# Kernel optimization log

Hardware: AMD Instinct MI355X
Metric: run time of the kernel (lower is better)

The kernel has to match this reference:

```python
import jax, jax.numpy as jnp
import numpy as np
from jax import lax

B, S, D, H, K = 2, 2048, 1024, 16, 3  # batch, seq, embed, heads, conv kernel
DEPTH = D // H


def silu(x):
    return x * jax.nn.sigmoid(x)


def sep_conv1d(x, dw, pw, b):
    """Keras SeparableConv1D, padding='same', activation=silu.
    x: [B,S,C]; dw: [K,1,C] depthwise kernel; pw: [C,F] pointwise; b: [F]."""
    C = x.shape[-1]
    y = lax.conv_general_dilated(
        x, dw, window_strides=(1,), padding='SAME',
        dimension_numbers=('NWC', 'WIO', 'NWC'), feature_group_count=C)
    y = jnp.einsum('bsc,cf->bsf', y, pw) + b
    return silu(y)


def setup_inputs() -> dict:
    key = jax.random.key(0)
    ks = jax.random.split(key, 20)
    sc = 1.0 / np.sqrt(D)
    inp = {
        'v': jax.random.normal(ks[0], (B, S, D), jnp.float32),
        'k': jax.random.normal(ks[1], (B, S, D), jnp.float32),
        'q': jax.random.normal(ks[2], (B, S, D), jnp.float32),
        'mask': jax.random.randint(ks[3], (B, 1, 1, S), 0, 2, jnp.int32),
        # Dense wq/wk/wv (SiLU)
        'wq_w': jax.random.normal(ks[4], (D, D), jnp.float32) * sc,
        'wq_b': jnp.zeros((D,), jnp.float32),
        'wk_w': jax.random.normal(ks[5], (D, D), jnp.float32) * sc,
        'wk_b': jnp.zeros((D,), jnp.float32),
        'wv_w': jax.random.normal(ks[6], (D, D), jnp.float32) * sc,
        'wv_b': jnp.zeros((D,), jnp.float32),
        # SeparableConv1D params (depthwise [K,1,D], pointwise [D,D], bias [D])
        'dwq': jax.random.normal(ks[7], (K, 1, D), jnp.float32) * 0.1,
        'pwq': jax.random.normal(ks[8], (D, D), jnp.float32) * sc,
        'bq': jnp.zeros((D,), jnp.float32),
        'dwk': jax.random.normal(ks[9], (K, 1, D), jnp.float32) * 0.1,
        'pwk': jax.random.normal(ks[10], (D, D), jnp.float32) * sc,
        'bk': jnp.zeros((D,), jnp.float32),
        'dwv': jax.random.normal(ks[11], (K, 1, D), jnp.float32) * 0.1,
        'pwv': jax.random.normal(ks[12], (D, D), jnp.float32) * sc,
        'bv': jnp.zeros((D,), jnp.float32),
        # output Dense (SiLU)
        'wo_w': jax.random.normal(ks[13], (D, D), jnp.float32) * sc,
        'wo_b': jnp.zeros((D,), jnp.float32),
    }
    return inp


def reference(v, k, q, mask, wq_w, wq_b, wk_w, wk_b, wv_w, wv_b,
              dwq, pwq, bq, dwk, pwk, bk, dwv, pwv, bv, wo_w, wo_b):
    # Dense projections with SiLU
    qp = silu(q @ wq_w + wq_b)
    kp = silu(k @ wk_w + wk_b)
    vp = silu(v @ wv_w + wv_b)
    # SeparableConv1D enhancements (SiLU)
    qc = sep_conv1d(qp, dwq, pwq, bq)
    kc = sep_conv1d(kp, dwk, pwk, bk)
    vc = sep_conv1d(vp, dwv, pwv, bv)
    # split heads -> [B,H,S,depth]
    def split(x):
        return x.reshape(B, S, H, DEPTH).transpose(0, 2, 1, 3)
    qh, kh, vh = split(qc), split(kc), split(vc)
    # scaled dot-product attention with additive mask penalty
    logits = jnp.einsum('bhqd,bhkd->bhqk', qh, kh) / jnp.sqrt(jnp.float32(DEPTH))
    logits = logits + mask.astype(jnp.float32) * -1e9
    attn = jax.nn.softmax(logits, axis=-1)
    out = jnp.einsum('bhqk,bhkd->bhqd', attn, vh)
    out = out.transpose(0, 2, 1, 3).reshape(B, S, D)
    return silu(out @ wo_w + wo_b)
```

## Files before the change

### kernel.cpp

```cpp
#include <hip/hip_runtime.h>
#include <hip/hip_fp16.h>
#include <math.h>

#define BB 2
#define SS 2048
#define DD 1024
#define HH 16
#define MTOT (BB*SS)

typedef _Float16 f16;
typedef _Float16 f16x4 __attribute__((ext_vector_type(4)));
typedef _Float16 f16x8 __attribute__((ext_vector_type(8)));
typedef float    f32x4 __attribute__((ext_vector_type(4)));

#define KSCALE 0.1803368801111204f

__device__ __forceinline__ float silu_f(float x) {
    return x / (1.0f + __expf(-x));
}

__device__ __forceinline__ void gload16(void* lds, const void* g) {
    __builtin_amdgcn_global_load_lds(
        (const __attribute__((address_space(1))) unsigned*)g,
        (__attribute__((address_space(3))) unsigned*)lds, 16, 0, 0);
}

__global__ __launch_bounds__(256) void prep(
    const float* __restrict__ q, const float* __restrict__ k, const float* __restrict__ v,
    f16* __restrict__ x0, f16* __restrict__ x1, f16* __restrict__ x2,
    const float* __restrict__ w0, const float* __restrict__ w1, const float* __restrict__ w2,
    const float* __restrict__ w3, const float* __restrict__ w4, const float* __restrict__ w5,
    const float* __restrict__ w6, f16* __restrict__ wt,
    const int* __restrict__ mask, int* __restrict__ uidx, int* __restrict__ ucnt)
{
    __shared__ float ts[64][65];
    const int gid = blockIdx.x;
    const int t = threadIdx.x;

    if (gid < 6144) {
        const int z = gid >> 11;
        const float* src = z == 0 ? q : z == 1 ? k : v;
        f16* dst = z == 0 ? x0 : z == 1 ? x1 : x2;
        const size_t i8 = ((size_t)(gid & 2047) * 256 + t) * 8;
        const float4 a = *(const float4*)(src + i8);
        const float4 b = *(const float4*)(src + i8 + 4);
        f16x8 h = {(f16)a.x,(f16)a.y,(f16)a.z,(f16)a.w,(f16)b.x,(f16)b.y,(f16)b.z,(f16)b.w};
        *(f16x8*)(dst + i8) = h;
    } else if (gid < 7936) {
        const int w = gid - 6144;
        const int z = w >> 8;
        const int rem = w & 255;
        const int bn = (rem & 15) << 6, bk = (rem >> 4) << 6;
        const float* src;
        switch (z) {
            case 0: src = w0; break; case 1: src = w1; break;
            case 2: src = w2; break; case 3: src = w3; break;
            case 4: src = w4; break; case 5: src = w5; break;
            default: src = w6; break;
        }
        f16* dst = wt + ((size_t)z << 20);
        #pragma unroll
        for (int i = 0; i < 4; ++i) {
            const int fid = t + (i << 8);
            const int r = fid >> 4, c4 = (fid & 15) << 2;
            const float4 v4 = *(const float4*)(src + (size_t)(bk + r) * 1024 + bn + c4);
            ts[r][c4 + 0] = v4.x; ts[r][c4 + 1] = v4.y;
            ts[r][c4 + 2] = v4.z; ts[r][c4 + 3] = v4.w;
        }
        __syncthreads();
        #pragma unroll
        for (int i = 0; i < 4; ++i) {
            const int fid = t + (i << 8);
            const int nr = fid >> 4, k4 = (fid & 15) << 2;
            f16x4 h = { (f16)ts[k4 + 0][nr], (f16)ts[k4 + 1][nr],
                        (f16)ts[k4 + 2][nr], (f16)ts[k4 + 3][nr] };
            *(f16x4*)(dst + (size_t)(bn + nr) * 1024 + bk + k4) = h;
        }
    } else {
        int* ps = (int*)ts;
        const int b = gid - 7936;
        int f[8]; int cnt = 0;
        const int base = b * SS + t * 8;
        #pragma unroll
        for (int j = 0; j < 8; ++j) { f[j] = (mask[base + j] == 0); cnt += f[j]; }
        ps[t] = cnt;
        __syncthreads();
        for (int off = 1; off < 256; off <<= 1) {
            const int pv = (t >= off) ? ps[t - off] : 0;
            __syncthreads();
            ps[t] += pv;
            __syncthreads();
        }
        int pos = ps[t] - cnt;
        #pragma unroll
        for (int j = 0; j < 8; ++j)
            if (f[j]) uidx[b * SS + pos++] = t * 8 + j;
        const int total = ps[255];
        const int pad = (total + 63) & ~63;
        for (int j = total + t; j < pad; j += 256) uidx[b * SS + j] = 0;
        if (t == 0) { ucnt[b * 2] = total; ucnt[b * 2 + 1] = pad; }
    }
}

__global__ __launch_bounds__(256) void dwconv3g(
    const f16* __restrict__ p0, const f16* __restrict__ p1, const f16* __restrict__ p2,
    const float* __restrict__ w0, const float* __restrict__ w1, const float* __restrict__ w2,
    f16* __restrict__ o0, f16* __restrict__ o1, f16* __restrict__ o2)
{
    const int z = blockIdx.y;
    const f16* x = z == 0 ? p0 : z == 1 ? p1 : p2;
    const float* dw = z == 0 ? w0 : z == 1 ? w1 : w2;
    f16* y = z == 0 ? o0 : z == 1 ? o1 : o2;
    const size_t i8 = ((size_t)blockIdx.x * 256 + threadIdx.x) * 8;
    const int c = (int)(i8 % DD);
    const int s = (int)((i8 / DD) % SS);
    const f16x8 xc = *(const f16x8*)(x + i8);
    float acc[8];
    #pragma unroll
    for (int j = 0; j < 8; ++j) acc[j] = (float)xc[j] * dw[DD + c + j];
    if (s > 0) {
        const f16x8 xm = *(const f16x8*)(x + i8 - DD);
        #pragma unroll
        for (int j = 0; j < 8; ++j) acc[j] = fmaf((float)xm[j], dw[c + j], acc[j]);
    }
    if (s < SS - 1) {
        const f16x8 xp = *(const f16x8*)(x + i8 + DD);
        #pragma unroll
        for (int j = 0; j < 8; ++j) acc[j] = fmaf((float)xp[j], dw[2 * DD + c + j], acc[j]);
    }
    f16x8 o;
    #pragma unroll
    for (int j = 0; j < 8; ++j) o[j] = (f16)acc[j];
    *(f16x8*)(y + i8) = o;
}

struct GArg { const f16* A; const f16* W; const float* b; void* C; float scale; };

template<int OUTF32>
__global__ __launch_bounds__(256) void gemm_f16(GArg g0, GArg g1, GArg g2)
{
    __shared__ f16 As[128 * 64];
    __shared__ f16 Bs[128 * 64];

    const GArg ga = blockIdx.z == 0 ? g0 : blockIdx.z == 1 ? g1 : g2;
    const int t = threadIdx.x, l = t & 63, wv = t >> 6;
    const int lr = l & 15, lg = l >> 4;
    const int wr = wv >> 1, wc = wv & 1;

    const int bid = blockIdx.y * 8 + blockIdx.x;
    const int sw = (bid & 7) * 32 + (bid >> 3);
    const int brow = (sw >> 3) << 7, bcol = (sw & 7) << 7;

    const int srow = l >> 3;
    const int schk = (l & 7) ^ (l >> 3);
    const f16* Abase = ga.A + (size_t)(brow + wv * 32 + srow) * 1024 + schk * 8;
    const f16* Bbase = ga.W + (size_t)(bcol + wv * 32 + srow) * 1024 + schk * 8;

    f32x4 acc[4][4];
    #pragma unroll
    for (int m = 0; m < 4; ++m)
        #pragma unroll
        for (int n = 0; n < 4; ++n) acc[m][n] = (f32x4){0.f, 0.f, 0.f, 0.f};

    for (int kt = 0; kt < 16; ++kt) {
        const int k0 = kt << 6;
        #pragma unroll
        for (int j = 0; j < 4; ++j) {
            gload16(As + (wv * 4 + j) * 512, Abase + (size_t)j * 8 * 1024 + k0);
            gload16(Bs + (wv * 4 + j) * 512, Bbase + (size_t)j * 8 * 1024 + k0);
        }
        __syncthreads();

        #pragma unroll
        for (int kk = 0; kk < 2; ++kk) {
            f16x8 af[4], bf[4];
            #pragma unroll
            for (int m = 0; m < 4; ++m) {
                const int row = (wr << 6) + (m << 4) + lr;
                const int off = row * 128 + ((((kk << 6) | (lg << 4))) ^ ((lr & 7) << 4));
                af[m] = *(const f16x8*)((const char*)As + off);
            }
            #pragma unroll
            for (int n = 0; n < 4; ++n) {
                const int row = (wc << 6) + (n << 4) + lr;
                const int off = row * 128 + ((((kk << 6) | (lg << 4))) ^ ((lr & 7) << 4));
                bf[n] = *(const f16x8*)((const char*)Bs + off);
            }
            #pragma unroll
            for (int m = 0; m < 4; ++m)
                #pragma unroll
                for (int n = 0; n < 4; ++n)
                    acc[m][n] = __builtin_amdgcn_mfma_f32_16x16x32_f16(af[m], bf[n], acc[m][n], 0, 0, 0);
        }
        __syncthreads();
    }

    float bv[4];
    #pragma unroll
    for (int n = 0; n < 4; ++n) bv[n] = ga.b[bcol + (wc << 6) + (n << 4) + lr];
    #pragma unroll
    for (int m = 0; m < 4; ++m)
        #pragma unroll
        for (int n = 0; n < 4; ++n)
            #pragma unroll
            for (int i = 0; i < 4; ++i) {
                const int row = brow + (wr << 6) + (m << 4) + (lg << 2) + i;
                const int col = bcol + (wc << 6) + (n << 4) + lr;
                const float o = silu_f(acc[m][n][i] + bv[n]) * ga.scale;
                if (OUTF32) ((float*)ga.C)[(size_t)row * 1024 + col] = o;
                else        ((f16*)ga.C)[(size_t)row * 1024 + col] = (f16)o;
            }
}

__global__ __launch_bounds__(512) void attn_f16(
    const f16* __restrict__ Q, const f16* __restrict__ Kf,
    const f16* __restrict__ Vf, const int* __restrict__ uidx,
    const int* __restrict__ ucnt, f16* __restrict__ O)
{
    __shared__ f16 Ks[64 * 64];
    __shared__ f16 Vt[64 * 64];
    __shared__ f16 Pw[8 * 16 * 64];
    __shared__ int uix[2048];

    const int t = threadIdx.x;
    const int l = t & 63, wv = t >> 6;
    const int lr = l & 15, lg = l >> 4;

    const int bid = blockIdx.x;
    const int sw = (bid & 7) * 32 + (bid >> 3);
    const int qb = (sw & 7) << 8;
    const int h  = (sw >> 3) & 15;
    const int b  = sw >> 7;

    const int cnt = ucnt[b * 2];
    const int pad = ucnt[b * 2 + 1];

    const int srow = l >> 3;
    const int schk = (l & 7) ^ (l >> 3);

    const int bkv = (t & 15) << 2;
    const int bnv = (t >> 4) << 2;

    for (int j = t; j < 2048; j += 512) uix[j] = uidx[b * SS + j];

    const size_t bbase = (size_t)b * SS;
    const size_t qrowA = bbase + qb + (wv << 4) + lr;
    const size_t qrowB = qrowA + 128;
    const f16x8 aqA0 = *(const f16x8*)(Q + qrowA * DD + h * 64 + (lg << 3));
    const f16x8 aqA1 = *(const f16x8*)(Q + qrowA * DD + h * 64 + 32 + (lg << 3));
    const f16x8 aqB0 = *(const f16x8*)(Q + qrowB * DD + h * 64 + (lg << 3));
    const f16x8 aqB1 = *(const f16x8*)(Q + qrowB * DD + h * 64 + 32 + (lg << 3));

    float mA[4], lA[4], mB[4], lB[4];
    f32x4 accA[4], accB[4];
    #pragma unroll
    for (int i = 0; i < 4; ++i) { mA[i] = -1e30f; lA[i] = 0.f; mB[i] = -1e30f; lB[i] = 0.f; }
    #pragma unroll
    for (int n = 0; n < 4; ++n) { accA[n] = (f32x4){0.f,0.f,0.f,0.f}; accB[n] = (f32x4){0.f,0.f,0.f,0.f}; }

    const int rdswz = (lr & 7) << 4;
    const int poff = (wv << 11) + lr * 128;

    __syncthreads();

#define PROCESS(AQ0, AQ1, M_, L_, ACC_) do {                                  \
    f32x4 s[4];                                                               \
    __builtin_amdgcn_s_setprio(1);                                            \
    _Pragma("unroll")                                                         \
    for (int n = 0; n < 4; ++n) {                                             \
        f32x4 z = (f32x4){0.f, 0.f, 0.f, 0.f};                                \
        z = __builtin_amdgcn_mfma_f32_16x16x32_f16(AQ0, bk0[n], z, 0, 0, 0);  \
        z = __builtin_amdgcn_mfma_f32_16x16x32_f16(AQ1, bk1[n], z, 0, 0, 0);  \
        if (full) {                                                           \
            _Pragma("unroll")                                                 \
            for (int i = 0; i < 4; ++i) s[n][i] = z[i];                       \
        } else {                                                              \
            const bool valid = (kt + (n << 4) + lr) < cnt;                    \
            _Pragma("unroll")                                                 \
            for (int i = 0; i < 4; ++i) s[n][i] = valid ? z[i] : -1e30f;      \
        }                                                                     \
    }                                                                         \
    __builtin_amdgcn_s_setprio(0);                                            \
    float pm[4];                                                              \
    _Pragma("unroll")                                                         \
    for (int i = 0; i < 4; ++i)                                               \
        pm[i] = fmaxf(fmaxf(s[0][i], s[1][i]), fmaxf(s[2][i], s[3][i]));      \
    float g = pm[0] - M_[0];                                                  \
    _Pragma("unroll")                                                         \
    for (int i = 1; i < 4; ++i) g = fmaxf(g, pm[i] - M_[i]);                  \
    if (!__all(g <= 8.0f)) {                 \
        float sc[4];                                                          \
        _Pragma("unroll")                                                     \
        for (int i = 0; i < 4; ++i) {                                         \
            float pr = pm[i];                                                 \
            pr = fmaxf(pr, __shfl_xor(pr, 1));                                \
            pr = fmaxf(pr, __shfl_xor(pr, 2));                                \
            pr = fmaxf(pr, __shfl_xor(pr, 4));                                \
            pr = fmaxf(pr, __shfl_xor(pr, 8));                                \
            const float mn = fmaxf(M_[i], pr);                                \
            sc[i] = exp2f(M_[i] - mn);                                        \
            M_[i] = mn;                                                       \
            L_[i] *= sc[i];                                                   \
        }                                                                     \
        _Pragma("unroll")                                                     \
        for (int n = 0; n < 4; ++n)                                           \
            _Pragma("unroll")                                                 \
            for (int i = 0; i < 4; ++i) ACC_[n][i] *= sc[i];                  \
    }                                                                         \
    _Pragma("unroll")                                                         \
    for (int n = 0; n < 4; ++n)                                               \
        _Pragma("unroll")                                                     \
        for (int i = 0; i < 4; ++i) {                                         \
            const float p = exp2f(s[n][i] - M_[i]);       \
            L_[i] += p;                                                       \
            const int row = (lg << 2) + i;                                    \
            const int off = (wv << 11) + row * 128 +                          \
                            ((((n << 4) + lr) * 2) ^ ((row & 7) << 4));       \
            *(f16*)((char*)Pw + off) = (f16)p;                                \
        }                                                                     \
    {                                                                         \
        const f16x8 pa0 = *(const f16x8*)((const char*)Pw + poff + (((lg << 4)) ^ rdswz));        \
        const f16x8 pa1 = *(const f16x8*)((const char*)Pw + poff + (((64) | (lg << 4)) ^ rdswz)); \
        __builtin_amdgcn_s_setprio(1);                                        \
        _Pragma("unroll")                                                     \
        for (int n = 0; n < 4; ++n) {                                         \
            const int row = (n << 4) + lr;                                    \
            const f16x8 bv0 = *(const f16x8*)((const char*)Vt + row * 128 + (((lg << 4)) ^ rdswz));        \
            const f16x8 bv1 = *(const f16x8*)((const char*)Vt + row * 128 + (((64) | (lg << 4)) ^ rdswz)); \
            ACC_[n] = __builtin_amdgcn_mfma_f32_16x16x32_f16(pa0, bv0, ACC_[n], 0, 0, 0);  \
            ACC_[n] = __builtin_amdgcn_mfma_f32_16x16x32_f16(pa1, bv1, ACC_[n], 0, 0, 0);  \
        }                                                                     \
        __builtin_amdgcn_s_setprio(0);                                        \
    }                                                                         \
} while (0)

    for (int kt = 0; kt < pad; kt += 64) {
        {
            const int krow = uix[kt + wv * 8 + srow];
            gload16(Ks + wv * 512, Kf + (bbase + krow) * DD + h * 64 + schk * 8);
        }
        if (t < 256) {
            f16x4 vl[4];
            #pragma unroll
            for (int r = 0; r < 4; ++r) {
                const int vrow = uix[kt + bkv + r];
                vl[r] = *(const f16x4*)(Vf + (bbase + vrow) * DD + h * 64 + bnv);
            }
            #pragma unroll
            for (int j = 0; j < 4; ++j) {
                f16x4 h4 = { vl[0][j], vl[1][j], vl[2][j], vl[3][j] };
                const int row = bnv + j;
                const int off = row * 128 + ((bkv * 2) ^ ((row & 7) << 4));
                *(f16x4*)((char*)Vt + off) = h4;
            }
        }
        __syncthreads();

        f16x8 bk0[4], bk1[4];
        #pragma unroll
        for (int n = 0; n < 4; ++n) {
            const int row = (n << 4) + lr;
            bk0[n] = *(const f16x8*)((const char*)Ks + row * 128 + (((lg << 4)) ^ rdswz));
            bk1[n] = *(const f16x8*)((const char*)Ks + row * 128 + (((64) | (lg << 4)) ^ rdswz));
        }
        const bool full = (kt + 64 <= cnt);

        PROCESS(aqA0, aqA1, mA, lA, accA);
        PROCESS(aqB0, aqB1, mB, lB, accB);

        __syncthreads();
    }
#undef PROCESS

    #pragma unroll
    for (int i = 0; i < 4; ++i) {
        lA[i] += __shfl_xor(lA[i], 1);
        lA[i] += __shfl_xor(lA[i], 2);
        lA[i] += __shfl_xor(lA[i], 4);
        lA[i] += __shfl_xor(lA[i], 8);
        lB[i] += __shfl_xor(lB[i], 1);
        lB[i] += __shfl_xor(lB[i], 2);
        lB[i] += __shfl_xor(lB[i], 4);
        lB[i] += __shfl_xor(lB[i], 8);
    }
    #pragma unroll
    for (int n = 0; n < 4; ++n)
        #pragma unroll
        for (int i = 0; i < 4; ++i) {
            const size_t rowA = bbase + qb + (wv << 4) + (lg << 2) + i;
            O[rowA * DD + h * 64 + (n << 4) + lr] = (f16)(accA[n][i] / lA[i]);
            O[(rowA + 128) * DD + h * 64 + (n << 4) + lr] = (f16)(accB[n][i] / lB[i]);
        }
}

extern "C" void kernel_launch(void* const* d_in, const int* in_sizes, int n_in,
                              void* d_out, int out_size, void* d_ws, size_t ws_size,
                              hipStream_t stream) {
    const float* v    = (const float*)d_in[0];
    const float* k    = (const float*)d_in[1];
    const float* q    = (const float*)d_in[2];
    const int*   mask = (const int*)  d_in[3];
    const float* wq_w = (const float*)d_in[4];
    const float* wq_b = (const float*)d_in[5];
    const float* wk_w = (const float*)d_in[6];
    const float* wk_b = (const float*)d_in[7];
    const float* wv_w = (const float*)d_in[8];
    const float* wv_b = (const float*)d_in[9];
    const float* dwq  = (const float*)d_in[10];
    const float* pwq  = (const float*)d_in[11];
    const float* bq   = (const float*)d_in[12];
    const float* dwk  = (const float*)d_in[13];
    const float* pwk  = (const float*)d_in[14];
    const float* bk   = (const float*)d_in[15];
    const float* dwv  = (const float*)d_in[16];
    const float* pwv  = (const float*)d_in[17];
    const float* bv   = (const float*)d_in[18];
    const float* wo_w = (const float*)d_in[19];
    const float* wo_b = (const float*)d_in[20];
    float* out = (float*)d_out;

    const size_t NE = (size_t)MTOT * DD;
    f16* wt = (f16*)d_ws;
    f16* x0 = wt + 7 * (size_t)(1 << 20);
    f16* x1 = x0 + NE;
    f16* x2 = x1 + NE;
    f16* p0 = x2 + NE;
    f16* p1 = p0 + NE;
    f16* p2 = p1 + NE;
    f16* ao = p2 + NE;
    int* uidx = (int*)(ao + NE);
    int* ucnt = uidx + MTOT;

    f16* wtq = wt,              *wtk = wt + (1u<<20), *wtv = wt + 2*(1u<<20);
    f16* wpq = wt + 3*(1u<<20), *wpk = wt + 4*(1u<<20), *wpv = wt + 5*(1u<<20);
    f16* wto = wt + 6*(1u<<20);

    prep<<<dim3(7938), 256, 0, stream>>>(q, k, v, x0, x1, x2,
        wq_w, wk_w, wv_w, pwq, pwk, pwv, wo_w, wt, mask, uidx, ucnt);
    gemm_f16<0><<<dim3(8, 32, 3), 256, 0, stream>>>(
        GArg{x0, wtq, wq_b, p0, 1.0f}, GArg{x1, wtk, wk_b, p1, 1.0f},
        GArg{x2, wtv, wv_b, p2, 1.0f});
    dwconv3g<<<dim3(2048, 3), 256, 0, stream>>>(p0, p1, p2, dwq, dwk, dwv, x0, x1, x2);
    gemm_f16<0><<<dim3(8, 32, 3), 256, 0, stream>>>(
        GArg{x0, wpq, bq, p0, 1.0f}, GArg{x1, wpk, bk, p1, KSCALE},
        GArg{x2, wpv, bv, p2, 1.0f});
    attn_f16<<<dim3(256), 512, 0, stream>>>(p0, p1, p2, uidx, ucnt, ao);
    gemm_f16<1><<<dim3(8, 32, 1), 256, 0, stream>>>(
        GArg{ao, wto, wo_b, out, 1.0f}, GArg{ao, wto, wo_b, out, 1.0f},
        GArg{ao, wto, wo_b, out, 1.0f});
}
```

Baseline: 203.4 us.

## Halve query rows per attention block, double grid, stage two KV tiles per sync

The attention kernel now gives each 512-thread block 128 query rows (one 16-row tile per wave) instead of 256, so the grid doubles to 512 blocks and fills more of the CUs. To keep LDS traffic and barrier count per key in check, each loop iteration now loads two 64-key K/V tiles into doubled shared buffers and processes both between one pair of barriers. Fewer query rows per block means each K/V tile is loaded from global memory twice as often overall, and the doubled LDS may limit how many blocks fit on a CU.

```diff
diff --git a/kernel.cpp b/kernel.cpp
--- a/kernel.cpp
+++ b/kernel.cpp
@@ -217,8 +217,8 @@
     const f16* __restrict__ Vf, const int* __restrict__ uidx,
     const int* __restrict__ ucnt, f16* __restrict__ O)
 {
-    __shared__ f16 Ks[64 * 64];
-    __shared__ f16 Vt[64 * 64];
+    __shared__ f16 Ks[2 * 64 * 64];
+    __shared__ f16 Vt[2 * 64 * 64];
     __shared__ f16 Pw[8 * 16 * 64];
     __shared__ int uix[2048];
 
@@ -227,10 +227,10 @@
     const int lr = l & 15, lg = l >> 4;
 
     const int bid = blockIdx.x;
-    const int sw = (bid & 7) * 32 + (bid >> 3);
-    const int qb = (sw & 7) << 8;
-    const int h  = (sw >> 3) & 15;
-    const int b  = sw >> 7;
+    const int sw = (bid & 7) * 64 + (bid >> 3);
+    const int qb = (sw & 15) << 7;
+    const int h  = (sw >> 4) & 15;
+    const int b  = sw >> 8;
 
     const int cnt = ucnt[b * 2];
     const int pad = ucnt[b * 2 + 1];
@@ -244,38 +244,44 @@
     for (int j = t; j < 2048; j += 512) uix[j] = uidx[b * SS + j];
 
     const size_t bbase = (size_t)b * SS;
-    const size_t qrowA = bbase + qb + (wv << 4) + lr;
-    const size_t qrowB = qrowA + 128;
-    const f16x8 aqA0 = *(const f16x8*)(Q + qrowA * DD + h * 64 + (lg << 3));
-    const f16x8 aqA1 = *(const f16x8*)(Q + qrowA * DD + h * 64 + 32 + (lg << 3));
-    const f16x8 aqB0 = *(const f16x8*)(Q + qrowB * DD + h * 64 + (lg << 3));
-    const f16x8 aqB1 = *(const f16x8*)(Q + qrowB * DD + h * 64 + 32 + (lg << 3));
-
-    float mA[4], lA[4], mB[4], lB[4];
-    f32x4 accA[4], accB[4];
-    #pragma unroll
-    for (int i = 0; i < 4; ++i) { mA[i] = -1e30f; lA[i] = 0.f; mB[i] = -1e30f; lB[i] = 0.f; }
-    #pragma unroll
-    for (int n = 0; n < 4; ++n) { accA[n] = (f32x4){0.f,0.f,0.f,0.f}; accB[n] = (f32x4){0.f,0.f,0.f,0.f}; }
+    const size_t qrow = bbase + qb + (wv << 4) + lr;
+    const f16x8 aq0 = *(const f16x8*)(Q + qrow * DD + h * 64 + (lg << 3));
+    const f16x8 aq1 = *(const f16x8*)(Q + qrow * DD + h * 64 + 32 + (lg << 3));
+
+    float m_i[4], l_i[4];
+    f32x4 acc[4];
+    #pragma unroll
+    for (int i = 0; i < 4; ++i) { m_i[i] = -1e30f; l_i[i] = 0.f; }
+    #pragma unroll
+    for (int n = 0; n < 4; ++n) acc[n] = (f32x4){0.f, 0.f, 0.f, 0.f};
 
     const int rdswz = (lr & 7) << 4;
     const int poff = (wv << 11) + lr * 128;
 
     __syncthreads();
 
-#define PROCESS(AQ0, AQ1, M_, L_, ACC_) do {                                  \
+#define PROCESS(TB, KT) do {                                                  \
+    const int kb = (TB) * 8192;                                               \
+    f16x8 bk0[4], bk1[4];                                                     \
+    _Pragma("unroll")                                                         \
+    for (int n = 0; n < 4; ++n) {                                             \
+        const int row = (n << 4) + lr;                                        \
+        bk0[n] = *(const f16x8*)((const char*)Ks + kb + row * 128 + (((lg << 4)) ^ rdswz));        \
+        bk1[n] = *(const f16x8*)((const char*)Ks + kb + row * 128 + (((64) | (lg << 4)) ^ rdswz)); \
+    }                                                                         \
+    const bool full = ((KT) + 64 <= cnt);                                     \
     f32x4 s[4];                                                               \
     __builtin_amdgcn_s_setprio(1);                                            \
     _Pragma("unroll")                                                         \
     for (int n = 0; n < 4; ++n) {                                             \
         f32x4 z = (f32x4){0.f, 0.f, 0.f, 0.f};                                \
-        z = __builtin_amdgcn_mfma_f32_16x16x32_f16(AQ0, bk0[n], z, 0, 0, 0);  \
-        z = __builtin_amdgcn_mfma_f32_16x16x32_f16(AQ1, bk1[n], z, 0, 0, 0);  \
+        z = __builtin_amdgcn_mfma_f32_16x16x32_f16(aq0, bk0[n], z, 0, 0, 0);  \
+        z = __builtin_amdgcn_mfma_f32_16x16x32_f16(aq1, bk1[n], z, 0, 0, 0);  \
         if (full) {                                                           \
             _Pragma("unroll")                                                 \
             for (int i = 0; i < 4; ++i) s[n][i] = z[i];                       \
         } else {                                                              \
-            const bool valid = (kt + (n << 4) + lr) < cnt;                    \
+            const bool valid = ((KT) + (n << 4) + lr) < cnt;                  \
             _Pragma("unroll")                                                 \
             for (int i = 0; i < 4; ++i) s[n][i] = valid ? z[i] : -1e30f;      \
         }                                                                     \
@@ -285,9 +291,9 @@
     _Pragma("unroll")                                                         \
     for (int i = 0; i < 4; ++i)                                               \
         pm[i] = fmaxf(fmaxf(s[0][i], s[1][i]), fmaxf(s[2][i], s[3][i]));      \
-    float g = pm[0] - M_[0];                                                  \
+    float g = pm[0] - m_i[0];                                                 \
     _Pragma("unroll")                                                         \
-    for (int i = 1; i < 4; ++i) g = fmaxf(g, pm[i] - M_[i]);                  \
+    for (int i = 1; i < 4; ++i) g = fmaxf(g, pm[i] - m_i[i]);                 \
     if (!__all(g <= 8.0f)) {                 \
         float sc[4];                                                          \
         _Pragma("unroll")                                                     \
@@ -297,22 +303,22 @@
             pr = fmaxf(pr, __shfl_xor(pr, 2));                                \
             pr = fmaxf(pr, __shfl_xor(pr, 4));                                \
             pr = fmaxf(pr, __shfl_xor(pr, 8));                                \
-            const float mn = fmaxf(M_[i], pr);                                \
-            sc[i] = exp2f(M_[i] - mn);                                        \
-            M_[i] = mn;                                                       \
-            L_[i] *= sc[i];                                                   \
+            const float mn = fmaxf(m_i[i], pr);                               \
+            sc[i] = exp2f(m_i[i] - mn);                                       \
+            m_i[i] = mn;                                                      \
+            l_i[i] *= sc[i];                                                  \
         }                                                                     \
         _Pragma("unroll")                                                     \
         for (int n = 0; n < 4; ++n)                                           \
             _Pragma("unroll")                                                 \
-            for (int i = 0; i < 4; ++i) ACC_[n][i] *= sc[i];                  \
+            for (int i = 0; i < 4; ++i) acc[n][i] *= sc[i];                   \
     }                                                                         \
     _Pragma("unroll")                                                         \
     for (int n = 0; n < 4; ++n)                                               \
         _Pragma("unroll")                                                     \
         for (int i = 0; i < 4; ++i) {                                         \
-            const float p = exp2f(s[n][i] - M_[i]);       \
-            L_[i] += p;                                                       \
+            const float p = exp2f(s[n][i] - m_i[i]);      \
+            l_i[i] += p;                                                      \
             const int row = (lg << 2) + i;                                    \
             const int off = (wv << 11) + row * 128 +                          \
                             ((((n << 4) + lr) * 2) ^ ((row & 7) << 4));       \
@@ -325,48 +331,47 @@
         _Pragma("unroll")                                                     \
         for (int n = 0; n < 4; ++n) {                                         \
             const int row = (n << 4) + lr;                                    \
-            const f16x8 bv0 = *(const f16x8*)((const char*)Vt + row * 128 + (((lg << 4)) ^ rdswz));        \
-            const f16x8 bv1 = *(const f16x8*)((const char*)Vt + row * 128 + (((64) | (lg << 4)) ^ rdswz)); \
-            ACC_[n] = __builtin_amdgcn_mfma_f32_16x16x32_f16(pa0, bv0, ACC_[n], 0, 0, 0);  \
-            ACC_[n] = __builtin_amdgcn_mfma_f32_16x16x32_f16(pa1, bv1, ACC_[n], 0, 0, 0);  \
+            const f16x8 bv0 = *(const f16x8*)((const char*)Vt + kb + row * 128 + (((lg << 4)) ^ rdswz));        \
+            const f16x8 bv1 = *(const f16x8*)((const char*)Vt + kb + row * 128 + (((64) | (lg << 4)) ^ rdswz)); \
+            acc[n] = __builtin_amdgcn_mfma_f32_16x16x32_f16(pa0, bv0, acc[n], 0, 0, 0);  \
+            acc[n] = __builtin_amdgcn_mfma_f32_16x16x32_f16(pa1, bv1, acc[n], 0, 0, 0);  \
         }                                                                     \
         __builtin_amdgcn_s_setprio(0);                                        \
     }                                                                         \
 } while (0)
 
-    for (int kt = 0; kt < pad; kt += 64) {
+    for (int kt = 0; kt < pad; kt += 128) {
+        const bool two = (kt + 64) < pad;
         {
-            const int krow = uix[kt + wv * 8 + srow];
-            gload16(Ks + wv * 512, Kf + (bbase + krow) * DD + h * 64 + schk * 8);
+            const int krow0 = uix[kt + wv * 8 + srow];
+            gload16(Ks + wv * 512, Kf + (bbase + krow0) * DD + h * 64 + schk * 8);
+            if (two) {
+                const int krow1 = uix[kt + 64 + wv * 8 + srow];
+                gload16(Ks + 4096 + wv * 512, Kf + (bbase + krow1) * DD + h * 64 + schk * 8);
+            }
         }
         if (t < 256) {
-            f16x4 vl[4];
-            #pragma unroll
-            for (int r = 0; r < 4; ++r) {
-                const int vrow = uix[kt + bkv + r];
-                vl[r] = *(const f16x4*)(Vf + (bbase + vrow) * DD + h * 64 + bnv);
+            const int nhalf = two ? 2 : 1;
+            for (int half = 0; half < nhalf; ++half) {
+                f16x4 vl[4];
+                #pragma unroll
+                for (int r = 0; r < 4; ++r) {
+                    const int vrow = uix[kt + half * 64 + bkv + r];
+                    vl[r] = *(const f16x4*)(Vf + (bbase + vrow) * DD + h * 64 + bnv);
+                }
+                #pragma unroll
+                for (int j = 0; j < 4; ++j) {
+                    f16x4 h4 = { vl[0][j], vl[1][j], vl[2][j], vl[3][j] };
+                    const int row = bnv + j;
+                    const int off = half * 8192 + row * 128 + ((bkv * 2) ^ ((row & 7) << 4));
+                    *(f16x4*)((char*)Vt + off) = h4;
+                }
             }
-            #pragma unroll
-            for (int j = 0; j < 4; ++j) {
-                f16x4 h4 = { vl[0][j], vl[1][j], vl[2][j], vl[3][j] };
-                const int row = bnv + j;
-                const int off = row * 128 + ((bkv * 2) ^ ((row & 7) << 4));
-                *(f16x4*)((char*)Vt + off) = h4;
-            }
-        }
-        __syncthreads();
-
-        f16x8 bk0[4], bk1[4];
-        #pragma unroll
-        for (int n = 0; n < 4; ++n) {
-            const int row = (n << 4) + lr;
-            bk0[n] = *(const f16x8*)((const char*)Ks + row * 128 + (((lg << 4)) ^ rdswz));
-            bk1[n] = *(const f16x8*)((const char*)Ks + row * 128 + (((64) | (lg << 4)) ^ rdswz));
-        }
-        const bool full = (kt + 64 <= cnt);
-
-        PROCESS(aqA0, aqA1, mA, lA, accA);
-        PROCESS(aqB0, aqB1, mB, lB, accB);
+        }
+        __syncthreads();
+
+        PROCESS(0, kt);
+        if (two) PROCESS(1, kt + 64);
 
         __syncthreads();
     }
@@ -374,22 +379,17 @@
 
     #pragma unroll
     for (int i = 0; i < 4; ++i) {
-        lA[i] += __shfl_xor(lA[i], 1);
-        lA[i] += __shfl_xor(lA[i], 2);
-        lA[i] += __shfl_xor(lA[i], 4);
-        lA[i] += __shfl_xor(lA[i], 8);
-        lB[i] += __shfl_xor(lB[i], 1);
-        lB[i] += __shfl_xor(lB[i], 2);
-        lB[i] += __shfl_xor(lB[i], 4);
-        lB[i] += __shfl_xor(lB[i], 8);
+        l_i[i] += __shfl_xor(l_i[i], 1);
+        l_i[i] += __shfl_xor(l_i[i], 2);
+        l_i[i] += __shfl_xor(l_i[i], 4);
+        l_i[i] += __shfl_xor(l_i[i], 8);
     }
     #pragma unroll
     for (int n = 0; n < 4; ++n)
         #pragma unroll
         for (int i = 0; i < 4; ++i) {
-            const size_t rowA = bbase + qb + (wv << 4) + (lg << 2) + i;
-            O[rowA * DD + h * 64 + (n << 4) + lr] = (f16)(accA[n][i] / lA[i]);
-            O[(rowA + 128) * DD + h * 64 + (n << 4) + lr] = (f16)(accB[n][i] / lB[i]);
+            const size_t row = bbase + qb + (wv << 4) + (lg << 2) + i;
+            O[row * DD + h * 64 + (n << 4) + lr] = (f16)(acc[n][i] / l_i[i]);
         }
 }
 
@@ -444,7 +444,7 @@
     gemm_f16<0><<<dim3(8, 32, 3), 256, 0, stream>>>(
         GArg{x0, wpq, bq, p0, 1.0f}, GArg{x1, wpk, bk, p1, KSCALE},
         GArg{x2, wpv, bv, p2, 1.0f});
-    attn_f16<<<dim3(256), 512, 0, stream>>>(p0, p1, p2, uidx, ucnt, ao);
+    attn_f16<<<dim3(512), 512, 0, stream>>>(p0, p1, p2, uidx, ucnt, ao);
     gemm_f16<1><<<dim3(8, 32, 1), 256, 0, stream>>>(
         GArg{ao, wto, wo_b, out, 1.0f}, GArg{ao, wto, wo_b, out, 1.0f},
         GArg{ao, wto, wo_b, out, 1.0f});
```

Result: faster. 196.4 us (-3.4%).
